# Optimization experiments

Measured on AMD Instinct MI355X. Metric: run time of the kernel, lower is better.

The kernel has to match this reference:

```python
import jax, jax.numpy as jnp
import numpy as np

IMG = 1280
STRIDES = (8, 16, 32)
ALPHA, GAMMA = 0.25, 2.0
OBJ_W, BOX_W, FOOT_W = 1.0, 5.0, 1.0
RADIUS, NUM_CAND, EPS = 2.5, 10, 1e-7


def _grid(H, W):
    ys, xs = jnp.meshgrid(jnp.arange(H, dtype=jnp.float32),
                          jnp.arange(W, dtype=jnp.float32), indexing='ij')
    return xs.reshape(-1), ys.reshape(-1)


def _iou_xyxy(a, b):
    lt = jnp.maximum(a[..., :2], b[..., :2])
    rb = jnp.minimum(a[..., 2:], b[..., 2:])
    wh = jnp.clip(rb - lt, 0.0)
    inter = wh[..., 0] * wh[..., 1]
    aa = (a[..., 2] - a[..., 0]) * (a[..., 3] - a[..., 1])
    ab = (b[..., 2] - b[..., 0]) * (b[..., 3] - b[..., 1])
    return inter / (aa + ab - inter + EPS)


def _assign_one(pred, gt_boxes, gt_foots, gt_valid, stride):
    # Faithful SimOTAAssigner.assign for one image/scale (torch @no_grad).
    pred = jax.lax.stop_gradient(pred)
    gt_boxes = jax.lax.stop_gradient(gt_boxes)
    gt_foots = jax.lax.stop_gradient(gt_foots)
    C, H, W = pred.shape
    HW = H * W
    gx, gy = _grid(H, W)
    s = stride / IMG
    p = pred.reshape(C, HW)
    obj_logit = p[0]
    pcx = (jax.nn.sigmoid(p[1]) + gx) * s
    pcy = (jax.nn.sigmoid(p[2]) + gy) * s
    pw = jnp.exp(jnp.clip(p[3], -5.0, 5.0)) * s
    ph = jnp.exp(jnp.clip(p[4], -5.0, 5.0)) * s
    pred_xyxy = jnp.stack([pcx - pw / 2, pcy - ph / 2, pcx + pw / 2, pcy + ph / 2], -1)
    cls_cost = jax.nn.softplus(-obj_logit)  # BCE_with_logits(logit, 1)
    cell = jnp.arange(HW)

    def step(carry, gt):
        obj_t, box_t, foot_t, pos_m = carry
        box, foot, valid = gt
        cx, cy, w, h = box[0], box[1], box[2], box[3]
        cxg, cyg = cx / s, cy / s
        in_center = (jnp.abs(gx - cxg) < RADIUS) & (jnp.abs(gy - cyg) < RADIUS)
        in_box = ((gx >= (cx - w / 2) / s) & (gx < (cx + w / 2) / s) &
                  (gy >= (cy - h / 2) / s) & (gy < (cy + h / 2) / s))
        cand = in_center | in_box
        dist = (gx - cxg) ** 2 + (gy - cyg) ** 2
        cand = jnp.where(jnp.any(cand), cand, cell == jnp.argmin(dist))
        gt_xyxy = jnp.stack([cx - w / 2, cy - h / 2, cx + w / 2, cy + h / 2])
        iou = _iou_xyxy(pred_xyxy, gt_xyxy)  # (HW,)
        cost = jnp.where(cand, cls_cost - 3.0 * jnp.log(iou + EPS), jnp.inf)
        n_cand = jnp.sum(cand)
        iou_sum = jnp.sum(jnp.where(cand, iou, 0.0))
        n_pos = jnp.clip(jnp.floor(iou_sum).astype(jnp.int32), 1,
                         jnp.minimum(NUM_CAND, n_cand))
        _, idx = jax.lax.top_k(-cost, NUM_CAND)
        sel = (jnp.arange(NUM_CAND) < n_pos) & valid
        best_iou = iou[idx[0]]  # pair_iou[topk_idx[0]] in the torch code
        pos_m = pos_m.at[idx].max(sel.astype(jnp.float32))
        obj_t = obj_t.at[idx].max(jnp.where(sel, best_iou, -jnp.inf))
        tx = cxg - gx[idx]
        ty = cyg - gy[idx]
        tw = jnp.log(w / s + EPS)
        th = jnp.log(h / s + EPS)
        new_box = jnp.stack([tx, ty, jnp.full_like(tx, tw), jnp.full_like(tx, th)], 0)
        box_t = box_t.at[:, idx].set(jnp.where(sel, new_box, box_t[:, idx]))
        new_foot = jnp.stack([jnp.full_like(tx, foot[0]), jnp.full_like(tx, foot[1])], 0)
        foot_t = foot_t.at[:, idx].set(jnp.where(sel, new_foot, foot_t[:, idx]))
        return (obj_t, box_t, foot_t, pos_m), None

    init = (jnp.zeros(HW), jnp.zeros((4, HW)), jnp.zeros((2, HW)), jnp.zeros(HW))
    (obj_t, box_t, foot_t, pos_m), _ = jax.lax.scan(
        step, init, (gt_boxes, gt_foots, gt_valid))
    return obj_t, box_t, foot_t, pos_m


def _ciou(pcx, pcy, pw, ph, tcx, tcy, tw, th):
    px1, py1, px2, py2 = pcx - pw / 2, pcy - ph / 2, pcx + pw / 2, pcy + ph / 2
    tx1, ty1, tx2, ty2 = tcx - tw / 2, tcy - th / 2, tcx + tw / 2, tcy + th / 2
    iw = jnp.clip(jnp.minimum(px2, tx2) - jnp.maximum(px1, tx1), 0.0)
    ih = jnp.clip(jnp.minimum(py2, ty2) - jnp.maximum(py1, ty1), 0.0)
    inter = iw * ih
    union = pw * ph + tw * th - inter + EPS
    iou = inter / union
    rho2 = (pcx - tcx) ** 2 + (pcy - tcy) ** 2
    cw = jnp.maximum(px2, tx2) - jnp.minimum(px1, tx1)
    ch = jnp.maximum(py2, ty2) - jnp.minimum(py1, ty1)
    c2 = cw ** 2 + ch ** 2 + EPS
    v = (4.0 / jnp.pi ** 2) * (jnp.arctan(tw / (th + EPS)) - jnp.arctan(pw / (ph + EPS))) ** 2
    alpha = jax.lax.stop_gradient(v / (1.0 - iou + v + EPS))
    return iou - rho2 / c2 - alpha * v


def _loss_one(pred, gt_boxes, gt_foots, gt_valid, stride):
    obj_t, box_t, foot_t, pm = _assign_one(pred, gt_boxes, gt_foots, gt_valid, stride)
    C, H, W = pred.shape
    HW = H * W
    p = pred.reshape(C, HW)
    gx, gy = _grid(H, W)
    s = stride / IMG
    # focal loss on objectness with soft IoU targets
    x, z = p[0], obj_t
    ce = jnp.maximum(x, 0.0) - x * z + jnp.log1p(jnp.exp(-jnp.abs(x)))
    prob = jax.nn.sigmoid(x)
    p_t = prob * z + (1.0 - prob) * (1.0 - z)
    a_t = ALPHA * z + (1.0 - ALPHA) * (1.0 - z)
    obj_loss = jnp.mean(a_t * (1.0 - p_t) ** GAMMA * ce)
    npos = jnp.maximum(jnp.sum(pm), 1.0)
    # CIoU box loss at positive cells (mask instead of gather, jit-friendly)
    pcx = (jax.nn.sigmoid(p[1]) + gx) * s
    pcy = (jax.nn.sigmoid(p[2]) + gy) * s
    pw = jnp.exp(jnp.clip(p[3], -5.0, 5.0)) * s
    ph = jnp.exp(jnp.clip(p[4], -5.0, 5.0)) * s
    tcx = (box_t[0] + gx) * s
    tcy = (box_t[1] + gy) * s
    tw = jnp.exp(box_t[2]) * s
    th = jnp.exp(box_t[3]) * s
    ciou = _ciou(pcx, pcy, pw, ph, tcx, tcy, tw, th)
    box_loss = jnp.sum(pm * (1.0 - ciou)) / npos
    # smooth-L1 foot loss on sigmoid-decoded foot point
    pf = jax.nn.sigmoid(p[5:7])
    d = jnp.abs(pf - foot_t)
    sl1 = jnp.where(d < 1.0, 0.5 * d * d, d - 0.5)
    foot_loss = jnp.sum(pm * jnp.sum(sl1, 0)) / npos
    return obj_loss, box_loss, foot_loss


def _forward(pred_s0, pred_s1, pred_s2, targets):
    B = pred_s0.shape[0]
    person = targets[..., 0] == 0  # person_mask; padded rows use cls != 0
    boxes = targets[..., 1:5]
    foots = targets[..., 5:7]
    size = jnp.maximum(boxes[..., 2], boxes[..., 3]) * IMG
    scale_masks = (size < 128.0, (size >= 48.0) & (size < 288.0), size >= 128.0)
    tot_obj = tot_box = tot_foot = 0.0
    for pred, stride, sm in zip((pred_s0, pred_s1, pred_s2), STRIDES, scale_masks):
        valid = person & sm
        o, bx, f = jax.vmap(_loss_one, in_axes=(0, 0, 0, 0, None))(
            pred, boxes, foots, valid, stride)
        tot_obj = tot_obj + jnp.sum(o)
        tot_box = tot_box + jnp.sum(bx)
        tot_foot = tot_foot + jnp.sum(f)
    return (OBJ_W * tot_obj + BOX_W * tot_box + FOOT_W * tot_foot) / B


def setup_inputs() -> dict:
    key = jax.random.key(0)
    ks = jax.random.split(key, 7)
    B, N = 64, 40
    pred_s0 = jax.random.normal(ks[0], (B, 7, 160, 160), jnp.float32)
    pred_s1 = jax.random.normal(ks[1], (B, 7, 80, 80), jnp.float32)
    pred_s2 = jax.random.normal(ks[2], (B, 7, 40, 40), jnp.float32)
    cls = (jax.random.uniform(ks[3], (B, N, 1)) > 0.9).astype(jnp.float32)
    cxy = jax.random.uniform(ks[4], (B, N, 2)) * 0.8 + 0.1
    wh = jax.random.uniform(ks[5], (B, N, 2)) * 0.28 + 0.01
    ft = jax.random.uniform(ks[6], (B, N, 2))
    targets = jnp.concatenate([cls, cxy, wh, ft], -1)
    return {"pred_s0": pred_s0, "pred_s1": pred_s1, "pred_s2": pred_s2,
            "targets": targets}


def reference(pred_s0, pred_s1, pred_s2, targets):
    return _forward(pred_s0, pred_s1, pred_s2, targets)
```

## Files before the change

kernel.cpp:

```cpp
#include <hip/hip_runtime.h>
#include <math.h>

#define NBATCH 64
#define NGT    40
#define HW0    25600
#define HW1    6400
#define HW2    1600
#define NTASK  (NBATCH*3*NGT)
#define NABLK  (NTASK/4)
#define MAXE   400
#define SENT   0xFFFFFFFFFFFFFFFFull
#define FEPS   1e-7f

__device__ __forceinline__ float frcp(float x){ return __builtin_amdgcn_rcpf(x); }
__device__ __forceinline__ float fsigm(float x){ return frcp(1.0f + __expf(-x)); }

__device__ __forceinline__ float focal0(float x){
  float e = __expf(-fabsf(x));
  float ce = fmaxf(x,0.0f) + __logf(1.0f+e);
  float prob = fsigm(x);
  return 0.75f*prob*prob*ce;
}
__device__ __forceinline__ float focalz(float x, float z){
  float e = __expf(-fabsf(x));
  float ce = fmaxf(x,0.0f) - x*z + __logf(1.0f+e);
  float prob = fsigm(x);
  float p_t = prob*z + (1.0f-prob)*(1.0f-z);
  float a_t = 0.25f*z + 0.75f*(1.0f-z);
  float om = 1.0f-p_t;
  return a_t*om*om*ce;
}

__device__ __forceinline__ unsigned long long shflx64(unsigned long long v, int m){
  int lo = __shfl_xor((int)(unsigned)(v & 0xFFFFFFFFull), m, 64);
  int hi = __shfl_xor((int)(unsigned)(v >> 32), m, 64);
  return (((unsigned long long)(unsigned)hi) << 32) | (unsigned)lo;
}
__device__ __forceinline__ float wredf(float v){
  #pragma unroll
  for (int o=32;o;o>>=1) v += __shfl_xor(v,o,64);
  return v;
}
__device__ __forceinline__ int wredi(int v){
  #pragma unroll
  for (int o=32;o;o>>=1) v += __shfl_xor(v,o,64);
  return v;
}
__device__ __forceinline__ unsigned long long wredmin64(unsigned long long v){
  #pragma unroll
  for (int o=32;o;o>>=1){ unsigned long long w = shflx64(v,o); v = (w<v)?w:v; }
  return v;
}

__device__ __forceinline__ float iou_of_cell_f(const float* __restrict__ P, int HW, int cell,
                                               int W, float s,
                                               float bx1, float by1, float bx2, float by2, float ab){
  int gy = cell / W;
  int gx = cell - gy*W;
  float gxf=(float)gx, gyf=(float)gy;
  float q1 = P[HW+cell], q2=P[2*HW+cell], q3=P[3*HW+cell], q4=P[4*HW+cell];
  float pcx = (fsigm(q1)+gxf)*s;
  float pcy = (fsigm(q2)+gyf)*s;
  float pw = __expf(fminf(fmaxf(q3,-5.0f),5.0f))*s;
  float ph = __expf(fminf(fmaxf(q4,-5.0f),5.0f))*s;
  float ax1=pcx-pw*0.5f, ay1=pcy-ph*0.5f, ax2=pcx+pw*0.5f, ay2=pcy+ph*0.5f;
  float ltx=fmaxf(ax1,bx1), lty=fmaxf(ay1,by1);
  float rbx=fminf(ax2,bx2), rby=fminf(ay2,by2);
  float iw=fmaxf(rbx-ltx,0.0f), ih=fmaxf(rby-lty,0.0f);
  float inter=iw*ih;
  float aa=(ax2-ax1)*(ay2-ay1);
  return inter*frcp(aa+ab-inter+FEPS);
}

__global__ __launch_bounds__(256) void k_assign(
    const float* __restrict__ p0, const float* __restrict__ p1,
    const float* __restrict__ p2, const float* __restrict__ tg,
    int2* __restrict__ meta, int* __restrict__ cells,
    float* __restrict__ ws_focal, float* __restrict__ out)
{
  if (blockIdx.x == 0 && threadIdx.x == 0) out[0] = 0.0f;
  int lane = threadIdx.x & 63;
  int wv   = threadIdx.x >> 6;
  int task = (blockIdx.x<<2) + wv;
  int g  = task % NGT;
  int bs = task / NGT;
  int sc = bs % 3;
  int b  = bs / 3;

  const float* tp = tg + (b*NGT + g)*7;
  float cls = tp[0], cx = tp[1], cy = tp[2], w = tp[3], h = tp[4];
  float sz = fmaxf(w,h)*1280.0f;
  bool valid = (cls == 0.0f);
  if (sc==0)      valid = valid && (sz < 128.0f);
  else if (sc==1) valid = valid && (sz >= 48.0f) && (sz < 288.0f);
  else            valid = valid && (sz >= 128.0f);

  int W, HW; float s; const float* P;
  if (sc==0)      { W=160; HW=HW0; s=8.0f/1280.0f;  P=p0; }
  else if (sc==1) { W=80;  HW=HW1; s=16.0f/1280.0f; P=p1; }
  else            { W=40;  HW=HW2; s=32.0f/1280.0f; P=p2; }
  P += (size_t)b*7*HW;

  if (!valid){
    if (lane==0) meta[task] = make_int2(0,0);
  } else {
    float inv_s = 1280.0f/(float)((sc==0)?8:(sc==1)?16:32);
    float cxg = cx*inv_s, cyg = cy*inv_s;
    float bx1 = cx - w*0.5f, bx2 = cx + w*0.5f;
    float by1 = cy - h*0.5f, by2 = cy + h*0.5f;
    float ab  = (bx2-bx1)*(by2-by1);
    float bxl = bx1*inv_s, bxr = bx2*inv_s, byt = by1*inv_s, byb = by2*inv_s;

    int x0 = max(0,   (int)floorf(fminf(cxg-2.5f, bxl)) - 1);
    int x1 = min(W-1, (int)floorf(fmaxf(cxg+2.5f, bxr)) + 1);
    int y0 = max(0,   (int)floorf(fminf(cyg-2.5f, byt)) - 1);
    int y1 = min(W-1, (int)floorf(fmaxf(cyg+2.5f, byb)) + 1);
    int rw = x1-x0+1, rh = y1-y0+1;
    int rn = rw*rh;

    unsigned long long t[10];
    #pragma unroll
    for (int j=0;j<10;++j) t[j]=SENT;
    int ncand = 0; float iousum = 0.0f;
    unsigned long long dmin = SENT;

    int rx = lane % rw, ry = lane / rw;
    int stepy = 64 / rw, stepx = 64 % rw;
    for (int r = lane; r < rn; r += 64){
      float gxf = (float)(x0+rx), gyf = (float)(y0+ry);
      int cell = (y0+ry)*W + (x0+rx);
      float q1 = P[HW+cell], q2 = P[2*HW+cell], q3 = P[3*HW+cell], q4 = P[4*HW+cell];
      float pcx = (fsigm(q1)+gxf)*s;
      float pcy = (fsigm(q2)+gyf)*s;
      float pw = __expf(fminf(fmaxf(q3,-5.0f),5.0f))*s;
      float ph = __expf(fminf(fmaxf(q4,-5.0f),5.0f))*s;
      float ax1 = pcx-pw*0.5f, ay1 = pcy-ph*0.5f, ax2 = pcx+pw*0.5f, ay2 = pcy+ph*0.5f;
      float ltx = fmaxf(ax1,bx1), lty = fmaxf(ay1,by1);
      float rbx = fminf(ax2,bx2), rby = fminf(ay2,by2);
      float iw = fmaxf(rbx-ltx,0.0f), ih = fmaxf(rby-lty,0.0f);
      float inter = iw*ih;
      float aa = (ax2-ax1)*(ay2-ay1);
      float iou = inter * frcp(aa+ab-inter+FEPS);
      bool ic = (fabsf(gxf-cxg)<2.5f) && (fabsf(gyf-cyg)<2.5f);
      bool ib = (gxf>=bxl)&&(gxf<bxr)&&(gyf>=byt)&&(gyf<byb);
      float dx = gxf-cxg, dy = gyf-cyg;
      float dist = dx*dx+dy*dy;
      unsigned long long dk = (((unsigned long long)__float_as_uint(dist))<<32)|(unsigned)cell;
      dmin = (dk<dmin)?dk:dmin;
      if (ic|ib){
        ncand += 1; iousum += iou;
        float q0 = P[cell];
        float ti = iou + FEPS;
        float ratio = (1.0f + __expf(-q0)) * frcp(ti*ti*ti);
        unsigned long long pk = (((unsigned long long)__float_as_uint(ratio))<<32)|(unsigned)cell;
        if (pk < t[9]){
          t[9] = pk;
          #pragma unroll
          for (int j=9;j>0;--j){ if (t[j]<t[j-1]){ unsigned long long tmp=t[j]; t[j]=t[j-1]; t[j-1]=tmp; } }
        }
      }
      rx += stepx; ry += stepy;
      if (rx >= rw){ rx -= rw; ry += 1; }
    }

    int NC = wredi(ncand);
    float IS = wredf(iousum);
    dmin = wredmin64(dmin);

    int npos, cell0;
    if (NC==0){
      npos = 1; cell0 = (int)(unsigned)dmin;
      if (lane==0) cells[task*10] = cell0;
    } else {
      int ub = NC < 10 ? NC : 10;
      int v = (int)floorf(IS);
      v = v < 1 ? 1 : v;
      npos = v > ub ? ub : v;
      int ptr = 0; cell0 = 0;
      for (int rd=0; rd<npos; ++rd){
        unsigned long long head = SENT;
        #pragma unroll
        for (int j=0;j<10;++j) head = (ptr==j)? t[j] : head;
        unsigned long long m = wredmin64(head);
        if (rd==0) cell0 = (int)(unsigned)m;
        if (lane==0) cells[task*10+rd] = (int)(unsigned)m;
        if (head==m && m!=SENT) ptr += 1;
      }
    }
    if (lane==0){
      float biou = iou_of_cell_f(P, HW, cell0, W, s, bx1, by1, bx2, by2, ab);
      meta[task] = make_int2(npos, __float_as_int(biou));
    }
  }

  float osum = 0.0f;
  {
    int chunk = blockIdx.x % 10;
    int n4c = (HW/10) >> 2;
    const float4* Q4 = (const float4*)P + chunk*n4c;
    for (int i = threadIdx.x; i < n4c; i += 256){
      float4 x4 = Q4[i];
      osum += focal0(x4.x) + focal0(x4.y) + focal0(x4.z) + focal0(x4.w);
    }
  }
  osum = wredf(osum);
  __shared__ float redf[4];
  if (lane==0) redf[wv] = osum;
  __syncthreads();
  if (threadIdx.x==0) ws_focal[blockIdx.x] = redf[0]+redf[1]+redf[2]+redf[3];
}

__global__ __launch_bounds__(512) void k_pos(
    const float* __restrict__ p0, const float* __restrict__ p1,
    const float* __restrict__ p2, const float* __restrict__ tg,
    const int2* __restrict__ meta, const int* __restrict__ cells,
    const float* __restrict__ ws_focal, float* __restrict__ out)
{
  __shared__ int   s_pack[MAXE];
  __shared__ float s_biou[MAXE];
  __shared__ int   s_cnt;
  __shared__ float red[4][8];

  int u = blockIdx.x;
  int b = u / 3, sc = u - b*3;
  int W, HW; float s; const float* P;
  if (sc==0)      { W=160; HW=HW0; s=8.0f/1280.0f;  P=p0; }
  else if (sc==1) { W=80;  HW=HW1; s=16.0f/1280.0f; P=p1; }
  else            { W=40;  HW=HW2; s=32.0f/1280.0f; P=p2; }
  P += (size_t)b*7*HW;

  if (threadIdx.x == 0) s_cnt = 0;
  __syncthreads();

  int tbase = u*NGT;
  if (threadIdx.x < NGT*10){
    int g = threadIdx.x / 10, sl = threadIdx.x - g*10;
    int2 m = meta[tbase + g];
    if (sl < m.x){
      int idx = atomicAdd(&s_cnt, 1);
      s_pack[idx] = (cells[(tbase+g)*10 + sl] << 6) | g;
      s_biou[idx] = __int_as_float(m.y);
    }
  }
  __syncthreads();
  int E = s_cnt;

  float osum = 0.0f, np = 0.0f, bsum = 0.0f, fsum = 0.0f;

  if (threadIdx.x < 10) osum = ws_focal[u*10 + threadIdx.x];

  if (threadIdx.x < E){
    int myp = s_pack[threadIdx.x];
    int mycell = myp >> 6;
    int pm = myp; float bm = s_biou[threadIdx.x];
    for (int j = 0; j < E; ++j){
      int p = s_pack[j];
      if ((p>>6) == mycell){
        pm = max(pm, p);
        bm = fmaxf(bm, s_biou[j]);
      }
    }
    if (pm == myp){
      np = 1.0f;
      int wg = myp & 63;
      float z = bm;
      int i = mycell;
      float x = P[i];
      osum += focalz(x, z) - focal0(x);
      const float* tpb = tg + (b*NGT + wg)*7;
      float cx=tpb[1], cy=tpb[2], w=tpb[3], h=tpb[4], fx=tpb[5], fy=tpb[6];
      int gyi = i / W;
      float gxf = (float)(i - gyi*W), gyf = (float)gyi;
      float pcx = (fsigm(P[HW+i])+gxf)*s;
      float pcy = (fsigm(P[2*HW+i])+gyf)*s;
      float pw = __expf(fminf(fmaxf(P[3*HW+i],-5.0f),5.0f))*s;
      float ph = __expf(fminf(fmaxf(P[4*HW+i],-5.0f),5.0f))*s;
      float tw = w + FEPS*s, th = h + FEPS*s;
      float px1=pcx-pw*0.5f, py1=pcy-ph*0.5f, px2=pcx+pw*0.5f, py2=pcy+ph*0.5f;
      float tx1=cx-tw*0.5f, ty1=cy-th*0.5f, tx2=cx+tw*0.5f, ty2=cy+th*0.5f;
      float iw = fmaxf(fminf(px2,tx2)-fmaxf(px1,tx1),0.0f);
      float ih = fmaxf(fminf(py2,ty2)-fmaxf(py1,ty1),0.0f);
      float inter = iw*ih;
      float uni = pw*ph + tw*th - inter + FEPS;
      float iou = inter/uni;
      float rho2 = (pcx-cx)*(pcx-cx)+(pcy-cy)*(pcy-cy);
      float cw = fmaxf(px2,tx2)-fminf(px1,tx1);
      float ch = fmaxf(py2,ty2)-fminf(py1,ty1);
      float c2 = cw*cw+ch*ch+FEPS;
      float da = atanf(tw/(th+FEPS)) - atanf(pw/(ph+FEPS));
      float v = (4.0f/(float)(M_PI*M_PI))*da*da;
      float alpha = v/(1.0f-iou+v+FEPS);
      float ciou = iou - rho2/c2 - alpha*v;
      bsum = 1.0f - ciou;
      float pf1 = fsigm(P[5*HW+i]);
      float pf2 = fsigm(P[6*HW+i]);
      float d1 = fabsf(pf1-fx), d2 = fabsf(pf2-fy);
      fsum = (d1<1.0f? 0.5f*d1*d1 : d1-0.5f) + (d2<1.0f? 0.5f*d2*d2 : d2-0.5f);
    }
  }

  int wv = threadIdx.x >> 6, lane = threadIdx.x & 63;
  osum = wredf(osum); np = wredf(np); bsum = wredf(bsum); fsum = wredf(fsum);
  if (lane==0){ red[0][wv]=osum; red[1][wv]=np; red[2][wv]=bsum; red[3][wv]=fsum; }
  __syncthreads();
  if (threadIdx.x==0){
    float a0=0,a1=0,a2=0,a3=0;
    #pragma unroll
    for (int j=0;j<8;++j){ a0+=red[0][j]; a1+=red[1][j]; a2+=red[2][j]; a3+=red[3][j]; }
    float hw = (float)HW;
    float npz = fmaxf(a1, 1.0f);
    float c = (a0/hw + 5.0f*a2/npz + a3/npz) * (1.0f/64.0f);
    atomicAdd(out, c);
  }
}

extern "C" void kernel_launch(void* const* d_in, const int* in_sizes, int n_in,
                              void* d_out, int out_size, void* d_ws, size_t ws_size,
                              hipStream_t stream) {
  (void)in_sizes; (void)n_in; (void)out_size; (void)ws_size;
  const float* p0 = (const float*)d_in[0];
  const float* p1 = (const float*)d_in[1];
  const float* p2 = (const float*)d_in[2];
  const float* tg = (const float*)d_in[3];

  int2*  meta     = (int2*)d_ws;
  int*   cells    = (int*)((char*)d_ws + (size_t)NTASK*8);
  float* ws_focal = (float*)((char*)d_ws + (size_t)NTASK*48);
  float* out      = (float*)d_out;

  k_assign<<<NABLK, 256, 0, stream>>>(p0, p1, p2, tg, meta, cells, ws_focal, out);
  k_pos   <<<NBATCH*3, 512, 0, stream>>>(p0, p1, p2, tg, meta, cells, ws_focal, out);
}
```

Before: 106.9 us.

## Fuse assignment and positive-loss kernels into one block per image-scale

Merges the per-GT assignment kernel and the per-(batch,scale) loss kernel into a single kernel with 1024-thread blocks, one block per image/scale. Each wavefront loops over GTs and writes its selected cells directly into shared memory instead of global workspace. The focal sum over the whole objectness map is now done by the same block. A small final kernel replaces the global atomicAdd. This removes a kernel launch and the global round-trip, but cuts the grid from 3840 waves-worth of blocks to 192 blocks, leaving heavy load imbalance on the scale-0 blocks and few blocks across the CUs.

```diff
diff --git a/kernel.cpp b/kernel.cpp
--- a/kernel.cpp
+++ b/kernel.cpp
@@ -6,8 +6,7 @@
 #define HW0    25600
 #define HW1    6400
 #define HW2    1600
-#define NTASK  (NBATCH*3*NGT)
-#define NABLK  (NTASK/4)
+#define NBLK   (NBATCH*3)
 #define MAXE   400
 #define SENT   0xFFFFFFFFFFFFFFFFull
 #define FEPS   1e-7f
@@ -72,39 +71,41 @@
   return inter*frcp(aa+ab-inter+FEPS);
 }
 
-__global__ __launch_bounds__(256) void k_assign(
+__global__ __launch_bounds__(1024) void k_fused(
     const float* __restrict__ p0, const float* __restrict__ p1,
     const float* __restrict__ p2, const float* __restrict__ tg,
-    int2* __restrict__ meta, int* __restrict__ cells,
-    float* __restrict__ ws_focal, float* __restrict__ out)
+    float* __restrict__ partials)
 {
-  if (blockIdx.x == 0 && threadIdx.x == 0) out[0] = 0.0f;
-  int lane = threadIdx.x & 63;
-  int wv   = threadIdx.x >> 6;
-  int task = (blockIdx.x<<2) + wv;
-  int g  = task % NGT;
-  int bs = task / NGT;
-  int sc = bs % 3;
-  int b  = bs / 3;
-
-  const float* tp = tg + (b*NGT + g)*7;
-  float cls = tp[0], cx = tp[1], cy = tp[2], w = tp[3], h = tp[4];
-  float sz = fmaxf(w,h)*1280.0f;
-  bool valid = (cls == 0.0f);
-  if (sc==0)      valid = valid && (sz < 128.0f);
-  else if (sc==1) valid = valid && (sz >= 48.0f) && (sz < 288.0f);
-  else            valid = valid && (sz >= 128.0f);
-
+  __shared__ int   s_pack[MAXE];
+  __shared__ float s_biou[MAXE];
+  __shared__ int   s_cnt;
+  __shared__ float red[4][16];
+
+  int u = blockIdx.x;
+  int b = u / 3, sc = u - b*3;
   int W, HW; float s; const float* P;
   if (sc==0)      { W=160; HW=HW0; s=8.0f/1280.0f;  P=p0; }
   else if (sc==1) { W=80;  HW=HW1; s=16.0f/1280.0f; P=p1; }
   else            { W=40;  HW=HW2; s=32.0f/1280.0f; P=p2; }
   P += (size_t)b*7*HW;
-
-  if (!valid){
-    if (lane==0) meta[task] = make_int2(0,0);
-  } else {
-    float inv_s = 1280.0f/(float)((sc==0)?8:(sc==1)?16:32);
+  float inv_s = 1280.0f/(float)((sc==0)?8:(sc==1)?16:32);
+
+  if (threadIdx.x == 0) s_cnt = 0;
+  __syncthreads();
+
+  int lane = threadIdx.x & 63;
+  int wv   = threadIdx.x >> 6;
+
+  for (int g = wv; g < NGT; g += 16){
+    const float* tp = tg + (b*NGT + g)*7;
+    float cls = tp[0], cx = tp[1], cy = tp[2], w = tp[3], h = tp[4];
+    float sz = fmaxf(w,h)*1280.0f;
+    bool valid = (cls == 0.0f);
+    if (sc==0)      valid = valid && (sz < 128.0f);
+    else if (sc==1) valid = valid && (sz >= 48.0f) && (sz < 288.0f);
+    else            valid = valid && (sz >= 128.0f);
+    if (!valid) continue;
+
     float cxg = cx*inv_s, cyg = cy*inv_s;
     float bx1 = cx - w*0.5f, bx2 = cx + w*0.5f;
     float by1 = cy - h*0.5f, by2 = cy + h*0.5f;
@@ -167,15 +168,22 @@
     float IS = wredf(iousum);
     dmin = wredmin64(dmin);
 
-    int npos, cell0;
-    if (NC==0){
-      npos = 1; cell0 = (int)(unsigned)dmin;
-      if (lane==0) cells[task*10] = cell0;
-    } else {
+    int npos;
+    if (NC==0) npos = 1;
+    else {
       int ub = NC < 10 ? NC : 10;
       int v = (int)floorf(IS);
       v = v < 1 ? 1 : v;
       npos = v > ub ? ub : v;
+    }
+    int idx = 0;
+    if (lane==0) idx = atomicAdd(&s_cnt, npos);
+
+    int cell0;
+    if (NC==0){
+      cell0 = (int)(unsigned)dmin;
+      if (lane==0) s_pack[idx] = (cell0<<6) | g;
+    } else {
       int ptr = 0; cell0 = 0;
       for (int rd=0; rd<npos; ++rd){
         unsigned long long head = SENT;
@@ -183,63 +191,13 @@
         for (int j=0;j<10;++j) head = (ptr==j)? t[j] : head;
         unsigned long long m = wredmin64(head);
         if (rd==0) cell0 = (int)(unsigned)m;
-        if (lane==0) cells[task*10+rd] = (int)(unsigned)m;
+        if (lane==0) s_pack[idx+rd] = (((int)(unsigned)m)<<6) | g;
         if (head==m && m!=SENT) ptr += 1;
       }
     }
     if (lane==0){
       float biou = iou_of_cell_f(P, HW, cell0, W, s, bx1, by1, bx2, by2, ab);
-      meta[task] = make_int2(npos, __float_as_int(biou));
-    }
-  }
-
-  float osum = 0.0f;
-  {
-    int chunk = blockIdx.x % 10;
-    int n4c = (HW/10) >> 2;
-    const float4* Q4 = (const float4*)P + chunk*n4c;
-    for (int i = threadIdx.x; i < n4c; i += 256){
-      float4 x4 = Q4[i];
-      osum += focal0(x4.x) + focal0(x4.y) + focal0(x4.z) + focal0(x4.w);
-    }
-  }
-  osum = wredf(osum);
-  __shared__ float redf[4];
-  if (lane==0) redf[wv] = osum;
-  __syncthreads();
-  if (threadIdx.x==0) ws_focal[blockIdx.x] = redf[0]+redf[1]+redf[2]+redf[3];
-}
-
-__global__ __launch_bounds__(512) void k_pos(
-    const float* __restrict__ p0, const float* __restrict__ p1,
-    const float* __restrict__ p2, const float* __restrict__ tg,
-    const int2* __restrict__ meta, const int* __restrict__ cells,
-    const float* __restrict__ ws_focal, float* __restrict__ out)
-{
-  __shared__ int   s_pack[MAXE];
-  __shared__ float s_biou[MAXE];
-  __shared__ int   s_cnt;
-  __shared__ float red[4][8];
-
-  int u = blockIdx.x;
-  int b = u / 3, sc = u - b*3;
-  int W, HW; float s; const float* P;
-  if (sc==0)      { W=160; HW=HW0; s=8.0f/1280.0f;  P=p0; }
-  else if (sc==1) { W=80;  HW=HW1; s=16.0f/1280.0f; P=p1; }
-  else            { W=40;  HW=HW2; s=32.0f/1280.0f; P=p2; }
-  P += (size_t)b*7*HW;
-
-  if (threadIdx.x == 0) s_cnt = 0;
-  __syncthreads();
-
-  int tbase = u*NGT;
-  if (threadIdx.x < NGT*10){
-    int g = threadIdx.x / 10, sl = threadIdx.x - g*10;
-    int2 m = meta[tbase + g];
-    if (sl < m.x){
-      int idx = atomicAdd(&s_cnt, 1);
-      s_pack[idx] = (cells[(tbase+g)*10 + sl] << 6) | g;
-      s_biou[idx] = __int_as_float(m.y);
+      for (int sl=0; sl<npos; ++sl) s_biou[idx+sl] = biou;
     }
   }
   __syncthreads();
@@ -247,7 +205,14 @@
 
   float osum = 0.0f, np = 0.0f, bsum = 0.0f, fsum = 0.0f;
 
-  if (threadIdx.x < 10) osum = ws_focal[u*10 + threadIdx.x];
+  {
+    const float4* P4 = (const float4*)P;
+    int n4 = HW >> 2;
+    for (int i = threadIdx.x; i < n4; i += 1024){
+      float4 x4 = P4[i];
+      osum += focal0(x4.x) + focal0(x4.y) + focal0(x4.z) + focal0(x4.w);
+    }
+  }
 
   if (threadIdx.x < E){
     int myp = s_pack[threadIdx.x];
@@ -299,19 +264,27 @@
     }
   }
 
-  int wv = threadIdx.x >> 6, lane = threadIdx.x & 63;
   osum = wredf(osum); np = wredf(np); bsum = wredf(bsum); fsum = wredf(fsum);
   if (lane==0){ red[0][wv]=osum; red[1][wv]=np; red[2][wv]=bsum; red[3][wv]=fsum; }
   __syncthreads();
   if (threadIdx.x==0){
     float a0=0,a1=0,a2=0,a3=0;
     #pragma unroll
-    for (int j=0;j<8;++j){ a0+=red[0][j]; a1+=red[1][j]; a2+=red[2][j]; a3+=red[3][j]; }
+    for (int j=0;j<16;++j){ a0+=red[0][j]; a1+=red[1][j]; a2+=red[2][j]; a3+=red[3][j]; }
     float hw = (float)HW;
     float npz = fmaxf(a1, 1.0f);
-    float c = (a0/hw + 5.0f*a2/npz + a3/npz) * (1.0f/64.0f);
-    atomicAdd(out, c);
+    partials[u] = a0/hw + 5.0f*a2/npz + a3/npz;
   }
+}
+
+__global__ void k_final(const float* __restrict__ partials, float* __restrict__ out){
+  int t = threadIdx.x;
+  float c = (t < NBLK) ? partials[t] : 0.0f;
+  c = wredf(c);
+  __shared__ float sh[4];
+  if ((t & 63) == 0) sh[t >> 6] = c;
+  __syncthreads();
+  if (t == 0) out[0] = (sh[0]+sh[1]+sh[2]+sh[3])*(1.0f/64.0f);
 }
 
 extern "C" void kernel_launch(void* const* d_in, const int* in_sizes, int n_in,
@@ -323,11 +296,9 @@
   const float* p2 = (const float*)d_in[2];
   const float* tg = (const float*)d_in[3];
 
-  int2*  meta     = (int2*)d_ws;
-  int*   cells    = (int*)((char*)d_ws + (size_t)NTASK*8);
-  float* ws_focal = (float*)((char*)d_ws + (size_t)NTASK*48);
+  float* partials = (float*)d_ws;
   float* out      = (float*)d_out;
 
-  k_assign<<<NABLK, 256, 0, stream>>>(p0, p1, p2, tg, meta, cells, ws_focal, out);
-  k_pos   <<<NBATCH*3, 512, 0, stream>>>(p0, p1, p2, tg, meta, cells, ws_focal, out);
-}
+  k_fused<<<NBLK, 1024, 0, stream>>>(p0, p1, p2, tg, partials);
+  k_final<<<1, 256, 0, stream>>>(partials, out);
+}
```

Result: slower. 109.5 us (+2.4%).
